# Kernel tuning notes

Measured on AMD Instinct MI355X. Metric: run time of the kernel, lower is better.

Reference implementation:

```python
import jax, jax.numpy as jnp
import numpy as np

N_EXPERTS = 8
N_ACTIVE = 2
DIM = 1024
HID = 2816
B, S = 4, 2048
W_SCALE = 0.02  # keep activations numerically tame


def setup_inputs() -> dict:
    key = jax.random.key(0)
    ks = jax.random.split(key, 9)
    return {
        "x": jax.random.normal(ks[0], (B, S, DIM), dtype=jnp.float32),
        "router_w": jax.random.normal(ks[1], (N_EXPERTS, DIM), dtype=jnp.float32) * W_SCALE,
        "expert_bias": jnp.zeros((N_EXPERTS,), dtype=jnp.float32),
        "gate_w": jax.random.normal(ks[2], (N_EXPERTS, HID, DIM), dtype=jnp.float32) * W_SCALE,
        "up_w": jax.random.normal(ks[3], (N_EXPERTS, HID, DIM), dtype=jnp.float32) * W_SCALE,
        "down_w": jax.random.normal(ks[4], (N_EXPERTS, DIM, HID), dtype=jnp.float32) * W_SCALE,
        "shared_gate_w": jax.random.normal(ks[5], (HID, DIM), dtype=jnp.float32) * W_SCALE,
        "shared_up_w": jax.random.normal(ks[6], (HID, DIM), dtype=jnp.float32) * W_SCALE,
        "shared_down_w": jax.random.normal(ks[7], (DIM, HID), dtype=jnp.float32) * W_SCALE,
    }


def _swiglu(x, gw, uw, dw):
    # x: [T, D]; gw/uw: [H, D]; dw: [D, H]
    return (jax.nn.silu(x @ gw.T) * (x @ uw.T)) @ dw.T


def reference(x, router_w, expert_bias, gate_w, up_w, down_w,
              shared_gate_w, shared_up_w, shared_down_w):
    bsz, seqlen, dim = x.shape
    x_flat = x.reshape(-1, dim)  # [T, D]

    # sigmoid router with auxfree bias, top-k selection
    logits = (x_flat @ router_w.T).astype(jnp.float32) + expert_bias  # [T, E]
    scores = jax.nn.sigmoid(logits)
    topk_scores, topk_idx = jax.lax.top_k(scores, N_ACTIVE)  # [T, K]
    topk_w = topk_scores / (jnp.sum(topk_scores, axis=-1, keepdims=True) + 1e-6)

    out = jnp.zeros_like(x_flat)
    # fixed small loop over experts; weight is 0 for unselected tokens,
    # which is mathematically identical to the masked gather/scatter in torch.
    for e in range(N_EXPERTS):
        w_e = jnp.sum(topk_w * (topk_idx == e), axis=-1)  # [T]
        y_e = _swiglu(x_flat, gate_w[e], up_w[e], down_w[e])  # [T, D]
        out = out + w_e[:, None].astype(x_flat.dtype) * y_e

    out = out + _swiglu(x_flat, shared_gate_w, shared_up_w, shared_down_w)
    return out.reshape(bsz, seqlen, dim)
```

## Files before the change

kernel.cpp:

```cpp
#include <hip/hip_runtime.h>
#include <hip/hip_bf16.h>
#include <stdint.h>

#define T_TOK  8192
#define DIM_   1024
#define HID_   2816
#define NEXP   8

typedef __bf16 bf16x8 __attribute__((ext_vector_type(8)));
typedef float  f32x4  __attribute__((ext_vector_type(4)));

__device__ __forceinline__ unsigned short f2bf(float f) {
  uint32_t u = __float_as_uint(f);
  u += 0x7FFFu + ((u >> 16) & 1u);
  return (unsigned short)(u >> 16);
}

__device__ __forceinline__ void gld_lds16(const void* g, void* l) {
  __builtin_amdgcn_global_load_lds(
      (const __attribute__((address_space(1))) uint32_t*)g,
      (__attribute__((address_space(3))) uint32_t*)l, 16, 0, 0);
}

__device__ __forceinline__ int lds_idx(int row, int col) {
  return row * 64 + ((((col >> 3) ^ (row & 7)) & 7) << 3);
}

__global__ __launch_bounds__(256) void cast_x_kernel(const float* __restrict__ in,
                                                     unsigned short* __restrict__ out) {
  int i = (blockIdx.x * 256 + threadIdx.x) * 8;
#pragma unroll
  for (int half = 0; half < 2; ++half) {
    float4 a = *reinterpret_cast<const float4*>(in + i + half * 4);
    ushort4 h4;
    h4.x = f2bf(a.x); h4.y = f2bf(a.y); h4.z = f2bf(a.z); h4.w = f2bf(a.w);
    *reinterpret_cast<ushort4*>(out + i + half * 4) = h4;
  }
}

__global__ __launch_bounds__(256) void cast_w_kernel(const float* __restrict__ in,
                                                     unsigned short* __restrict__ out) {
  size_t i = ((size_t)blockIdx.x * 256 + threadIdx.x) * 8;
#pragma unroll
  for (int half = 0; half < 2; ++half) {
    float4 a = *reinterpret_cast<const float4*>(in + i + half * 4);
    ushort4 h4;
    h4.x = f2bf(a.x); h4.y = f2bf(a.y); h4.z = f2bf(a.z); h4.w = f2bf(a.w);
    *reinterpret_cast<ushort4*>(out + i + half * 4) = h4;
  }
}

__global__ __launch_bounds__(256) void router_kernel(
    const float* __restrict__ x, const float* __restrict__ rw,
    const float* __restrict__ bias, int* __restrict__ cnt,
    int* __restrict__ list, float* __restrict__ wlist) {
  __shared__ float rws[NEXP * DIM_];
  for (int i = threadIdx.x; i < NEXP * DIM_ / 4; i += 256)
    reinterpret_cast<float4*>(rws)[i] = reinterpret_cast<const float4*>(rw)[i];
  __syncthreads();
  int wave = threadIdx.x >> 6, lane = threadIdx.x & 63;
  int t = blockIdx.x * 4 + wave;
  const float* xr = x + (size_t)t * DIM_;
  float p[NEXP];
#pragma unroll
  for (int e = 0; e < NEXP; ++e) p[e] = 0.f;
  for (int i = 0; i < DIM_ / 64; ++i) {
    float xv = xr[i * 64 + lane];
#pragma unroll
    for (int e = 0; e < NEXP; ++e) p[e] += xv * rws[e * DIM_ + i * 64 + lane];
  }
#pragma unroll
  for (int e = 0; e < NEXP; ++e) {
#pragma unroll
    for (int s = 32; s > 0; s >>= 1) p[e] += __shfl_xor(p[e], s);
  }
  if (lane == 0) {
    float sc[NEXP];
#pragma unroll
    for (int e = 0; e < NEXP; ++e) sc[e] = 1.f / (1.f + __expf(-(p[e] + bias[e])));
    int e0 = 0; float s0 = sc[0];
#pragma unroll
    for (int e = 1; e < NEXP; ++e) if (sc[e] > s0) { s0 = sc[e]; e0 = e; }
    int e1 = -1; float s1 = -1.f;
#pragma unroll
    for (int e = 0; e < NEXP; ++e) if (e != e0 && sc[e] > s1) { s1 = sc[e]; e1 = e; }
    float inv = 1.f / (s0 + s1 + 1e-6f);
    int p0 = atomicAdd(&cnt[e0], 1);
    list[e0 * T_TOK + p0] = t; wlist[e0 * T_TOK + p0] = s0 * inv;
    int p1 = atomicAdd(&cnt[e1], 1);
    list[e1 * T_TOK + p1] = t; wlist[e1 * T_TOK + p1] = s1 * inv;
  }
}

__global__ void scan_kernel(const int* __restrict__ cnt, int* __restrict__ off) {
  if (threadIdx.x == 0) {
    int a = 0;
#pragma unroll
    for (int e = 0; e < NEXP; ++e) { off[e] = a; a += cnt[e]; }
  }
}

template <bool EXPERT, bool WBF16>
__global__ __launch_bounds__(512) void gateup_k(
    const unsigned short* __restrict__ xbf,
    const void* __restrict__ gw_, const void* __restrict__ uw_,
    const int* __restrict__ cnt, const int* __restrict__ off,
    const int* __restrict__ list, unsigned short* __restrict__ hout) {
  const int e = EXPERT ? blockIdx.z : 0;
  const int cnt_e = EXPERT ? cnt[e] : T_TOK;
  const int bn = blockIdx.x, mb = blockIdx.y;
  if (mb * 128 >= cnt_e) return;
  const int rowoff = EXPERT ? off[e] : 0;

  __shared__ unsigned short As[128 * 64];
  __shared__ unsigned short Bg[128 * 64];
  __shared__ unsigned short Bu[128 * 64];

  const int tid = threadIdx.x;
  const size_t eoff = EXPERT ? (size_t)e * HID_ * DIM_ : 0;
  const unsigned short* gwb = WBF16 ? (const unsigned short*)gw_ + eoff : nullptr;
  const unsigned short* uwb = WBF16 ? (const unsigned short*)uw_ + eoff : nullptr;
  const float* gwf = WBF16 ? nullptr : (const float*)gw_ + eoff;
  const float* uwf = WBF16 ? nullptr : (const float*)uw_ + eoff;

  size_t arow[2], brow[2];
#pragma unroll
  for (int j = 0; j < 2; ++j) {
    int c = tid + j * 512;
    int r = c >> 3;
    int u = (c & 7) ^ (r & 7);
    int rl = mb * 128 + r;
    int gr;
    if (EXPERT) { int cl = rl < cnt_e ? rl : cnt_e - 1; gr = list[e * T_TOK + cl]; }
    else gr = rl;
    arow[j] = (size_t)gr * DIM_ + (size_t)(u * 8);
    brow[j] = (size_t)(bn * 128 + r) * DIM_ + (size_t)(u * 8);
  }
  size_t brow4[4];
  int bwr4[4];
  if (!WBF16) {
#pragma unroll
    for (int j = 0; j < 4; ++j) {
      int f = tid + j * 512;
      int rb = f >> 4, s = f & 15;
      bwr4[j] = rb * 64 + (((s >> 1) ^ (rb & 7)) * 2 + (s & 1)) * 4;
      brow4[j] = (size_t)(bn * 128 + rb) * DIM_ + (size_t)(s * 4);
    }
  }

  const f32x4 vzero = {0.f, 0.f, 0.f, 0.f};
  f32x4 accg[4][2], accu[4][2];
#pragma unroll
  for (int m = 0; m < 4; ++m)
#pragma unroll
    for (int n = 0; n < 2; ++n) { accg[m][n] = vzero; accu[m][n] = vzero; }

  const int wid = tid >> 6, lane = tid & 63;
  const int wm = wid >> 2, wn = wid & 3;
  const int fr = lane & 15, fk = (lane >> 4) * 8;

  for (int k0 = 0; k0 < DIM_; k0 += 64) {
    __syncthreads();
#pragma unroll
    for (int j = 0; j < 2; ++j) {
      int c = tid + j * 512;
      gld_lds16(xbf + arow[j] + k0, &As[c * 8]);
      if (WBF16) {
        gld_lds16(gwb + brow[j] + k0, &Bg[c * 8]);
        gld_lds16(uwb + brow[j] + k0, &Bu[c * 8]);
      }
    }
    if (!WBF16) {
#pragma unroll
      for (int j = 0; j < 4; ++j) {
        float4 vg = *reinterpret_cast<const float4*>(gwf + brow4[j] + k0);
        float4 vu = *reinterpret_cast<const float4*>(uwf + brow4[j] + k0);
        ushort4 wg; wg.x = f2bf(vg.x); wg.y = f2bf(vg.y); wg.z = f2bf(vg.z); wg.w = f2bf(vg.w);
        ushort4 wu; wu.x = f2bf(vu.x); wu.y = f2bf(vu.y); wu.z = f2bf(vu.z); wu.w = f2bf(vu.w);
        *reinterpret_cast<ushort4*>(&Bg[bwr4[j]]) = wg;
        *reinterpret_cast<ushort4*>(&Bu[bwr4[j]]) = wu;
      }
    }
    __syncthreads();
#pragma unroll
    for (int kk = 0; kk < 64; kk += 32) {
      bf16x8 a[4], bg[2], bu[2];
#pragma unroll
      for (int m = 0; m < 4; ++m) {
        int ar = wm * 64 + m * 16 + fr;
        a[m] = *reinterpret_cast<const bf16x8*>(&As[lds_idx(ar, kk + fk)]);
      }
#pragma unroll
      for (int n = 0; n < 2; ++n) {
        int br = wn * 32 + n * 16 + fr;
        bg[n] = *reinterpret_cast<const bf16x8*>(&Bg[lds_idx(br, kk + fk)]);
        bu[n] = *reinterpret_cast<const bf16x8*>(&Bu[lds_idx(br, kk + fk)]);
      }
#pragma unroll
      for (int m = 0; m < 4; ++m)
#pragma unroll
        for (int n = 0; n < 2; ++n) {
          accg[m][n] = __builtin_amdgcn_mfma_f32_16x16x32_bf16(a[m], bg[n], accg[m][n], 0, 0, 0);
          accu[m][n] = __builtin_amdgcn_mfma_f32_16x16x32_bf16(a[m], bu[n], accu[m][n], 0, 0, 0);
        }
    }
  }

  const int rb = mb * 128 + wm * 64 + (lane >> 4) * 4;
  const int cb = bn * 128 + wn * 32 + fr;
#pragma unroll
  for (int m = 0; m < 4; ++m) {
#pragma unroll
    for (int r = 0; r < 4; ++r) {
      int rl = rb + m * 16 + r;
      if (EXPERT && rl >= cnt_e) continue;
      size_t rowbase = (size_t)(rowoff + rl) * HID_ + cb;
#pragma unroll
      for (int n = 0; n < 2; ++n) {
        float g = accg[m][n][r], u = accu[m][n][r];
        float hv = (g / (1.f + __expf(-g))) * u;
        hout[rowbase + n * 16] = f2bf(hv);
      }
    }
  }
}

template <bool EXPERT, bool WBF16>
__global__ __launch_bounds__(512) void down_k(
    const unsigned short* __restrict__ h, const void* __restrict__ dw_,
    const int* __restrict__ cnt, const int* __restrict__ off,
    const int* __restrict__ list, const float* __restrict__ wlist,
    float* __restrict__ out) {
  const int e = EXPERT ? blockIdx.z : 0;
  const int cnt_e = EXPERT ? cnt[e] : T_TOK;
  const int bn = blockIdx.x, mb = blockIdx.y;
  if (mb * 128 >= cnt_e) return;
  const int rowoff = EXPERT ? off[e] : 0;

  __shared__ unsigned short As[128 * 64];
  __shared__ unsigned short Bs[128 * 64];

  const int tid = threadIdx.x;
  const size_t eoff = EXPERT ? (size_t)e * DIM_ * HID_ : 0;
  const unsigned short* dwb = WBF16 ? (const unsigned short*)dw_ + eoff : nullptr;
  const float* dwf = WBF16 ? nullptr : (const float*)dw_ + eoff;

  size_t arow[2], brow[2];
#pragma unroll
  for (int j = 0; j < 2; ++j) {
    int c = tid + j * 512;
    int r = c >> 3;
    int u = (c & 7) ^ (r & 7);
    int rl = mb * 128 + r;
    int cl = (EXPERT && rl >= cnt_e) ? cnt_e - 1 : rl;
    arow[j] = (size_t)(rowoff + cl) * HID_ + (size_t)(u * 8);
    brow[j] = (size_t)(bn * 128 + r) * HID_ + (size_t)(u * 8);
  }
  size_t brow4[4];
  int bwr4[4];
  if (!WBF16) {
#pragma unroll
    for (int j = 0; j < 4; ++j) {
      int f = tid + j * 512;
      int rb = f >> 4, s = f & 15;
      bwr4[j] = rb * 64 + (((s >> 1) ^ (rb & 7)) * 2 + (s & 1)) * 4;
      brow4[j] = (size_t)(bn * 128 + rb) * HID_ + (size_t)(s * 4);
    }
  }

  const f32x4 vzero = {0.f, 0.f, 0.f, 0.f};
  f32x4 acc[4][2];
#pragma unroll
  for (int m = 0; m < 4; ++m)
#pragma unroll
    for (int n = 0; n < 2; ++n) acc[m][n] = vzero;

  const int wid = tid >> 6, lane = tid & 63;
  const int wm = wid >> 2, wn = wid & 3;
  const int fr = lane & 15, fk = (lane >> 4) * 8;

  for (int k0 = 0; k0 < HID_; k0 += 64) {
    __syncthreads();
#pragma unroll
    for (int j = 0; j < 2; ++j) {
      int c = tid + j * 512;
      gld_lds16(h + arow[j] + k0, &As[c * 8]);
      if (WBF16) gld_lds16(dwb + brow[j] + k0, &Bs[c * 8]);
    }
    if (!WBF16) {
#pragma unroll
      for (int j = 0; j < 4; ++j) {
        float4 v = *reinterpret_cast<const float4*>(dwf + brow4[j] + k0);
        ushort4 w; w.x = f2bf(v.x); w.y = f2bf(v.y); w.z = f2bf(v.z); w.w = f2bf(v.w);
        *reinterpret_cast<ushort4*>(&Bs[bwr4[j]]) = w;
      }
    }
    __syncthreads();
#pragma unroll
    for (int kk = 0; kk < 64; kk += 32) {
      bf16x8 a[4], b[2];
#pragma unroll
      for (int m = 0; m < 4; ++m) {
        int ar = wm * 64 + m * 16 + fr;
        a[m] = *reinterpret_cast<const bf16x8*>(&As[lds_idx(ar, kk + fk)]);
      }
#pragma unroll
      for (int n = 0; n < 2; ++n) {
        int br = wn * 32 + n * 16 + fr;
        b[n] = *reinterpret_cast<const bf16x8*>(&Bs[lds_idx(br, kk + fk)]);
      }
#pragma unroll
      for (int m = 0; m < 4; ++m)
#pragma unroll
        for (int n = 0; n < 2; ++n)
          acc[m][n] = __builtin_amdgcn_mfma_f32_16x16x32_bf16(a[m], b[n], acc[m][n], 0, 0, 0);
    }
  }

  const int rb = mb * 128 + wm * 64 + (lane >> 4) * 4;
  const int cb = bn * 128 + wn * 32 + fr;
#pragma unroll
  for (int m = 0; m < 4; ++m) {
#pragma unroll
    for (int r = 0; r < 4; ++r) {
      int rl = rb + m * 16 + r;
      if (EXPERT && rl >= cnt_e) continue;
      int tok; float w;
      if (EXPERT) { tok = list[e * T_TOK + rl]; w = wlist[e * T_TOK + rl]; }
      else { tok = rl; w = 1.f; }
      float* orow = out + (size_t)tok * DIM_ + cb;
#pragma unroll
      for (int n = 0; n < 2; ++n)
        atomicAdd(orow + n * 16, w * acc[m][n][r]);
    }
  }
}

extern "C" void kernel_launch(void* const* d_in, const int* in_sizes, int n_in,
                              void* d_out, int out_size, void* d_ws, size_t ws_size,
                              hipStream_t stream) {
  const float* x    = (const float*)d_in[0];
  const float* rw   = (const float*)d_in[1];
  const float* bias = (const float*)d_in[2];
  const float* gw   = (const float*)d_in[3];
  const float* uw   = (const float*)d_in[4];
  const float* dwn  = (const float*)d_in[5];
  const float* sgw  = (const float*)d_in[6];
  const float* suw  = (const float*)d_in[7];
  const float* sdw  = (const float*)d_in[8];
  float* out = (float*)d_out;

  char* ws = (char*)d_ws;
  size_t o = 0;
  auto alloc = [&](size_t b) { size_t r = o; o = (o + b + 255) & ~(size_t)255; return r; };
  unsigned short* xbf = (unsigned short*)(ws + alloc((size_t)T_TOK * DIM_ * 2));
  unsigned short* h   = (unsigned short*)(ws + alloc(((size_t)2 * T_TOK + 128) * HID_ * 2));
  int*   cnt   = (int*)(ws + alloc(NEXP * 4));
  int*   off   = (int*)(ws + alloc(NEXP * 4));
  int*   list  = (int*)(ws + alloc((size_t)NEXP * T_TOK * 4));
  float* wlist = (float*)(ws + alloc((size_t)NEXP * T_TOK * 4));
  const size_t need_base = o;
  const size_t WE = (size_t)HID_ * DIM_;
  unsigned short* gwb  = (unsigned short*)(ws + alloc(NEXP * WE * 2));
  unsigned short* uwb  = (unsigned short*)(ws + alloc(NEXP * WE * 2));
  const bool pcGU = (o <= ws_size);
  unsigned short* dwb  = (unsigned short*)(ws + alloc(NEXP * WE * 2));
  const bool pcDN = (o <= ws_size);
  unsigned short* sgwb = (unsigned short*)(ws + alloc(WE * 2));
  unsigned short* suwb = (unsigned short*)(ws + alloc(WE * 2));
  unsigned short* sdwb = (unsigned short*)(ws + alloc(WE * 2));
  const bool pcSH = (o <= ws_size);
  if (need_base > ws_size) {
    hipMemsetAsync(d_out, 0, (size_t)out_size * 4, stream);
    return;
  }

  hipMemsetAsync(out, 0, (size_t)out_size * 4, stream);
  hipMemsetAsync(cnt, 0, NEXP * 4, stream);
  cast_x_kernel<<<T_TOK * DIM_ / 8 / 256, 256, 0, stream>>>(x, xbf);
  router_kernel<<<T_TOK / 4, 256, 0, stream>>>(x, rw, bias, cnt, list, wlist);
  scan_kernel<<<1, 64, 0, stream>>>(cnt, off);

  const int WB = (int)(NEXP * WE / 2048);
  const int WS = (int)(WE / 2048);
  if (pcGU) {
    cast_w_kernel<<<WB, 256, 0, stream>>>(gw, gwb);
    cast_w_kernel<<<WB, 256, 0, stream>>>(uw, uwb);
  }
  if (pcDN) cast_w_kernel<<<WB, 256, 0, stream>>>(dwn, dwb);
  if (pcSH) {
    cast_w_kernel<<<WS, 256, 0, stream>>>(sgw, sgwb);
    cast_w_kernel<<<WS, 256, 0, stream>>>(suw, suwb);
    cast_w_kernel<<<WS, 256, 0, stream>>>(sdw, sdwb);
  }

  if (pcSH) {
    gateup_k<false, true><<<dim3(HID_ / 128, T_TOK / 128, 1), 512, 0, stream>>>(
        xbf, sgwb, suwb, cnt, off, list, h);
    down_k<false, true><<<dim3(DIM_ / 128, T_TOK / 128, 1), 512, 0, stream>>>(
        h, sdwb, cnt, off, list, wlist, out);
  } else {
    gateup_k<false, false><<<dim3(HID_ / 128, T_TOK / 128, 1), 512, 0, stream>>>(
        xbf, sgw, suw, cnt, off, list, h);
    down_k<false, false><<<dim3(DIM_ / 128, T_TOK / 128, 1), 512, 0, stream>>>(
        h, sdw, cnt, off, list, wlist, out);
  }
  if (pcGU)
    gateup_k<true, true><<<dim3(HID_ / 128, T_TOK / 128, NEXP), 512, 0, stream>>>(
        xbf, gwb, uwb, cnt, off, list, h);
  else
    gateup_k<true, false><<<dim3(HID_ / 128, T_TOK / 128, NEXP), 512, 0, stream>>>(
        xbf, gw, uw, cnt, off, list, h);
  if (pcDN)
    down_k<true, true><<<dim3(DIM_ / 128, T_TOK / 128, NEXP), 512, 0, stream>>>(
        h, dwb, cnt, off, list, wlist, out);
  else
    down_k<true, false><<<dim3(DIM_ / 128, T_TOK / 128, NEXP), 512, 0, stream>>>(
        h, dwn, cnt, off, list, wlist, out);
}
```

Measured before the change: 1.086 ms.

## Widen GEMM N-tiles to 256, drop fp32 weight fallback, store shared output directly

The gate/up kernel now runs 1024-thread blocks covering 256 hidden columns per tile, and the down kernel covers 256 output columns with a 4x4 fragment tile per wave. The goal is more reuse of each loaded A tile and fewer blocks. The shared-expert down pass writes its output with plain stores instead of atomics, which also removes the memset of the output. The fp32-weight fallback paths are removed, so the kernel now requires enough workspace for all bf16 weight copies. The cost is higher LDS and register use per block, which may lower occupancy.

```diff
diff --git a/kernel.cpp b/kernel.cpp
--- a/kernel.cpp
+++ b/kernel.cpp
@@ -100,10 +100,10 @@
   }
 }
 
-template <bool EXPERT, bool WBF16>
-__global__ __launch_bounds__(512) void gateup_k(
+template <bool EXPERT>
+__global__ __launch_bounds__(1024) void gateup_k(
     const unsigned short* __restrict__ xbf,
-    const void* __restrict__ gw_, const void* __restrict__ uw_,
+    const unsigned short* __restrict__ gwb_, const unsigned short* __restrict__ uwb_,
     const int* __restrict__ cnt, const int* __restrict__ off,
     const int* __restrict__ list, unsigned short* __restrict__ hout) {
   const int e = EXPERT ? blockIdx.z : 0;
@@ -113,39 +113,32 @@
   const int rowoff = EXPERT ? off[e] : 0;
 
   __shared__ unsigned short As[128 * 64];
-  __shared__ unsigned short Bg[128 * 64];
-  __shared__ unsigned short Bu[128 * 64];
+  __shared__ unsigned short Bg[256 * 64];
+  __shared__ unsigned short Bu[256 * 64];
 
   const int tid = threadIdx.x;
   const size_t eoff = EXPERT ? (size_t)e * HID_ * DIM_ : 0;
-  const unsigned short* gwb = WBF16 ? (const unsigned short*)gw_ + eoff : nullptr;
-  const unsigned short* uwb = WBF16 ? (const unsigned short*)uw_ + eoff : nullptr;
-  const float* gwf = WBF16 ? nullptr : (const float*)gw_ + eoff;
-  const float* uwf = WBF16 ? nullptr : (const float*)uw_ + eoff;
-
-  size_t arow[2], brow[2];
-#pragma unroll
-  for (int j = 0; j < 2; ++j) {
-    int c = tid + j * 512;
+  const unsigned short* gwb = gwb_ + eoff;
+  const unsigned short* uwb = uwb_ + eoff;
+
+  size_t arow;
+  {
+    int c = tid;
     int r = c >> 3;
     int u = (c & 7) ^ (r & 7);
     int rl = mb * 128 + r;
     int gr;
     if (EXPERT) { int cl = rl < cnt_e ? rl : cnt_e - 1; gr = list[e * T_TOK + cl]; }
     else gr = rl;
-    arow[j] = (size_t)gr * DIM_ + (size_t)(u * 8);
-    brow[j] = (size_t)(bn * 128 + r) * DIM_ + (size_t)(u * 8);
-  }
-  size_t brow4[4];
-  int bwr4[4];
-  if (!WBF16) {
-#pragma unroll
-    for (int j = 0; j < 4; ++j) {
-      int f = tid + j * 512;
-      int rb = f >> 4, s = f & 15;
-      bwr4[j] = rb * 64 + (((s >> 1) ^ (rb & 7)) * 2 + (s & 1)) * 4;
-      brow4[j] = (size_t)(bn * 128 + rb) * DIM_ + (size_t)(s * 4);
-    }
+    arow = (size_t)gr * DIM_ + (size_t)(u * 8);
+  }
+  size_t brow[2];
+#pragma unroll
+  for (int j = 0; j < 2; ++j) {
+    int c = tid + j * 1024;
+    int r = c >> 3;
+    int u = (c & 7) ^ (r & 7);
+    brow[j] = (size_t)(bn * 256 + r) * DIM_ + (size_t)(u * 8);
   }
 
   const f32x4 vzero = {0.f, 0.f, 0.f, 0.f};
@@ -156,30 +149,17 @@
     for (int n = 0; n < 2; ++n) { accg[m][n] = vzero; accu[m][n] = vzero; }
 
   const int wid = tid >> 6, lane = tid & 63;
-  const int wm = wid >> 2, wn = wid & 3;
+  const int wm = wid >> 3, wn = wid & 7;
   const int fr = lane & 15, fk = (lane >> 4) * 8;
 
   for (int k0 = 0; k0 < DIM_; k0 += 64) {
     __syncthreads();
+    gld_lds16(xbf + arow + k0, &As[tid * 8]);
 #pragma unroll
     for (int j = 0; j < 2; ++j) {
-      int c = tid + j * 512;
-      gld_lds16(xbf + arow[j] + k0, &As[c * 8]);
-      if (WBF16) {
-        gld_lds16(gwb + brow[j] + k0, &Bg[c * 8]);
-        gld_lds16(uwb + brow[j] + k0, &Bu[c * 8]);
-      }
-    }
-    if (!WBF16) {
-#pragma unroll
-      for (int j = 0; j < 4; ++j) {
-        float4 vg = *reinterpret_cast<const float4*>(gwf + brow4[j] + k0);
-        float4 vu = *reinterpret_cast<const float4*>(uwf + brow4[j] + k0);
-        ushort4 wg; wg.x = f2bf(vg.x); wg.y = f2bf(vg.y); wg.z = f2bf(vg.z); wg.w = f2bf(vg.w);
-        ushort4 wu; wu.x = f2bf(vu.x); wu.y = f2bf(vu.y); wu.z = f2bf(vu.z); wu.w = f2bf(vu.w);
-        *reinterpret_cast<ushort4*>(&Bg[bwr4[j]]) = wg;
-        *reinterpret_cast<ushort4*>(&Bu[bwr4[j]]) = wu;
-      }
+      int c = tid + j * 1024;
+      gld_lds16(gwb + brow[j] + k0, &Bg[c * 8]);
+      gld_lds16(uwb + brow[j] + k0, &Bu[c * 8]);
     }
     __syncthreads();
 #pragma unroll
@@ -207,7 +187,7 @@
   }
 
   const int rb = mb * 128 + wm * 64 + (lane >> 4) * 4;
-  const int cb = bn * 128 + wn * 32 + fr;
+  const int cb = bn * 256 + wn * 32 + fr;
 #pragma unroll
   for (int m = 0; m < 4; ++m) {
 #pragma unroll
@@ -225,9 +205,9 @@
   }
 }
 
-template <bool EXPERT, bool WBF16>
+template <bool EXPERT>
 __global__ __launch_bounds__(512) void down_k(
-    const unsigned short* __restrict__ h, const void* __restrict__ dw_,
+    const unsigned short* __restrict__ h, const unsigned short* __restrict__ dwb_,
     const int* __restrict__ cnt, const int* __restrict__ off,
     const int* __restrict__ list, const float* __restrict__ wlist,
     float* __restrict__ out) {
@@ -238,14 +218,12 @@
   const int rowoff = EXPERT ? off[e] : 0;
 
   __shared__ unsigned short As[128 * 64];
-  __shared__ unsigned short Bs[128 * 64];
+  __shared__ unsigned short Bs[256 * 64];
 
   const int tid = threadIdx.x;
-  const size_t eoff = EXPERT ? (size_t)e * DIM_ * HID_ : 0;
-  const unsigned short* dwb = WBF16 ? (const unsigned short*)dw_ + eoff : nullptr;
-  const float* dwf = WBF16 ? nullptr : (const float*)dw_ + eoff;
-
-  size_t arow[2], brow[2];
+  const unsigned short* dwb = dwb_ + (EXPERT ? (size_t)e * DIM_ * HID_ : 0);
+
+  size_t arow[2];
 #pragma unroll
   for (int j = 0; j < 2; ++j) {
     int c = tid + j * 512;
@@ -254,26 +232,22 @@
     int rl = mb * 128 + r;
     int cl = (EXPERT && rl >= cnt_e) ? cnt_e - 1 : rl;
     arow[j] = (size_t)(rowoff + cl) * HID_ + (size_t)(u * 8);
-    brow[j] = (size_t)(bn * 128 + r) * HID_ + (size_t)(u * 8);
-  }
-  size_t brow4[4];
-  int bwr4[4];
-  if (!WBF16) {
-#pragma unroll
-    for (int j = 0; j < 4; ++j) {
-      int f = tid + j * 512;
-      int rb = f >> 4, s = f & 15;
-      bwr4[j] = rb * 64 + (((s >> 1) ^ (rb & 7)) * 2 + (s & 1)) * 4;
-      brow4[j] = (size_t)(bn * 128 + rb) * HID_ + (size_t)(s * 4);
-    }
+  }
+  size_t brow[4];
+#pragma unroll
+  for (int j = 0; j < 4; ++j) {
+    int c = tid + j * 512;
+    int r = c >> 3;
+    int u = (c & 7) ^ (r & 7);
+    brow[j] = (size_t)(bn * 256 + r) * HID_ + (size_t)(u * 8);
   }
 
   const f32x4 vzero = {0.f, 0.f, 0.f, 0.f};
-  f32x4 acc[4][2];
+  f32x4 acc[4][4];
 #pragma unroll
   for (int m = 0; m < 4; ++m)
 #pragma unroll
-    for (int n = 0; n < 2; ++n) acc[m][n] = vzero;
+    for (int n = 0; n < 4; ++n) acc[m][n] = vzero;
 
   const int wid = tid >> 6, lane = tid & 63;
   const int wm = wid >> 2, wn = wid & 3;
@@ -285,53 +259,55 @@
     for (int j = 0; j < 2; ++j) {
       int c = tid + j * 512;
       gld_lds16(h + arow[j] + k0, &As[c * 8]);
-      if (WBF16) gld_lds16(dwb + brow[j] + k0, &Bs[c * 8]);
-    }
-    if (!WBF16) {
-#pragma unroll
-      for (int j = 0; j < 4; ++j) {
-        float4 v = *reinterpret_cast<const float4*>(dwf + brow4[j] + k0);
-        ushort4 w; w.x = f2bf(v.x); w.y = f2bf(v.y); w.z = f2bf(v.z); w.w = f2bf(v.w);
-        *reinterpret_cast<ushort4*>(&Bs[bwr4[j]]) = w;
-      }
+    }
+#pragma unroll
+    for (int j = 0; j < 4; ++j) {
+      int c = tid + j * 512;
+      gld_lds16(dwb + brow[j] + k0, &Bs[c * 8]);
     }
     __syncthreads();
 #pragma unroll
     for (int kk = 0; kk < 64; kk += 32) {
-      bf16x8 a[4], b[2];
+      bf16x8 a[4], b[4];
 #pragma unroll
       for (int m = 0; m < 4; ++m) {
         int ar = wm * 64 + m * 16 + fr;
         a[m] = *reinterpret_cast<const bf16x8*>(&As[lds_idx(ar, kk + fk)]);
       }
 #pragma unroll
-      for (int n = 0; n < 2; ++n) {
-        int br = wn * 32 + n * 16 + fr;
+      for (int n = 0; n < 4; ++n) {
+        int br = wn * 64 + n * 16 + fr;
         b[n] = *reinterpret_cast<const bf16x8*>(&Bs[lds_idx(br, kk + fk)]);
       }
 #pragma unroll
       for (int m = 0; m < 4; ++m)
 #pragma unroll
-        for (int n = 0; n < 2; ++n)
+        for (int n = 0; n < 4; ++n)
           acc[m][n] = __builtin_amdgcn_mfma_f32_16x16x32_bf16(a[m], b[n], acc[m][n], 0, 0, 0);
     }
   }
 
   const int rb = mb * 128 + wm * 64 + (lane >> 4) * 4;
-  const int cb = bn * 128 + wn * 32 + fr;
+  const int cb = bn * 256 + wn * 64 + fr;
 #pragma unroll
   for (int m = 0; m < 4; ++m) {
 #pragma unroll
     for (int r = 0; r < 4; ++r) {
       int rl = rb + m * 16 + r;
       if (EXPERT && rl >= cnt_e) continue;
-      int tok; float w;
-      if (EXPERT) { tok = list[e * T_TOK + rl]; w = wlist[e * T_TOK + rl]; }
-      else { tok = rl; w = 1.f; }
-      float* orow = out + (size_t)tok * DIM_ + cb;
-#pragma unroll
-      for (int n = 0; n < 2; ++n)
-        atomicAdd(orow + n * 16, w * acc[m][n][r]);
+      if (EXPERT) {
+        int tok = list[e * T_TOK + rl];
+        float w = wlist[e * T_TOK + rl];
+        float* orow = out + (size_t)tok * DIM_ + cb;
+#pragma unroll
+        for (int n = 0; n < 4; ++n)
+          atomicAdd(orow + n * 16, w * acc[m][n][r]);
+      } else {
+        float* orow = out + (size_t)rl * DIM_ + cb;
+#pragma unroll
+        for (int n = 0; n < 4; ++n)
+          orow[n * 16] = acc[m][n][r];
+      }
     }
   }
 }
@@ -359,23 +335,18 @@
   int*   off   = (int*)(ws + alloc(NEXP * 4));
   int*   list  = (int*)(ws + alloc((size_t)NEXP * T_TOK * 4));
   float* wlist = (float*)(ws + alloc((size_t)NEXP * T_TOK * 4));
-  const size_t need_base = o;
   const size_t WE = (size_t)HID_ * DIM_;
   unsigned short* gwb  = (unsigned short*)(ws + alloc(NEXP * WE * 2));
   unsigned short* uwb  = (unsigned short*)(ws + alloc(NEXP * WE * 2));
-  const bool pcGU = (o <= ws_size);
   unsigned short* dwb  = (unsigned short*)(ws + alloc(NEXP * WE * 2));
-  const bool pcDN = (o <= ws_size);
   unsigned short* sgwb = (unsigned short*)(ws + alloc(WE * 2));
   unsigned short* suwb = (unsigned short*)(ws + alloc(WE * 2));
   unsigned short* sdwb = (unsigned short*)(ws + alloc(WE * 2));
-  const bool pcSH = (o <= ws_size);
-  if (need_base > ws_size) {
+  if (o > ws_size) {
     hipMemsetAsync(d_out, 0, (size_t)out_size * 4, stream);
     return;
   }
 
-  hipMemsetAsync(out, 0, (size_t)out_size * 4, stream);
   hipMemsetAsync(cnt, 0, NEXP * 4, stream);
   cast_x_kernel<<<T_TOK * DIM_ / 8 / 256, 256, 0, stream>>>(x, xbf);
   router_kernel<<<T_TOK / 4, 256, 0, stream>>>(x, rw, bias, cnt, list, wlist);
@@ -383,38 +354,19 @@
 
   const int WB = (int)(NEXP * WE / 2048);
   const int WS = (int)(WE / 2048);
-  if (pcGU) {
-    cast_w_kernel<<<WB, 256, 0, stream>>>(gw, gwb);
-    cast_w_kernel<<<WB, 256, 0, stream>>>(uw, uwb);
-  }
-  if (pcDN) cast_w_kernel<<<WB, 256, 0, stream>>>(dwn, dwb);
-  if (pcSH) {
-    cast_w_kernel<<<WS, 256, 0, stream>>>(sgw, sgwb);
-    cast_w_kernel<<<WS, 256, 0, stream>>>(suw, suwb);
-    cast_w_kernel<<<WS, 256, 0, stream>>>(sdw, sdwb);
-  }
-
-  if (pcSH) {
-    gateup_k<false, true><<<dim3(HID_ / 128, T_TOK / 128, 1), 512, 0, stream>>>(
-        xbf, sgwb, suwb, cnt, off, list, h);
-    down_k<false, true><<<dim3(DIM_ / 128, T_TOK / 128, 1), 512, 0, stream>>>(
-        h, sdwb, cnt, off, list, wlist, out);
-  } else {
-    gateup_k<false, false><<<dim3(HID_ / 128, T_TOK / 128, 1), 512, 0, stream>>>(
-        xbf, sgw, suw, cnt, off, list, h);
-    down_k<false, false><<<dim3(DIM_ / 128, T_TOK / 128, 1), 512, 0, stream>>>(
-        h, sdw, cnt, off, list, wlist, out);
-  }
-  if (pcGU)
-    gateup_k<true, true><<<dim3(HID_ / 128, T_TOK / 128, NEXP), 512, 0, stream>>>(
-        xbf, gwb, uwb, cnt, off, list, h);
-  else
-    gateup_k<true, false><<<dim3(HID_ / 128, T_TOK / 128, NEXP), 512, 0, stream>>>(
-        xbf, gw, uw, cnt, off, list, h);
-  if (pcDN)
-    down_k<true, true><<<dim3(DIM_ / 128, T_TOK / 128, NEXP), 512, 0, stream>>>(
-        h, dwb, cnt, off, list, wlist, out);
-  else
-    down_k<true, false><<<dim3(DIM_ / 128, T_TOK / 128, NEXP), 512, 0, stream>>>(
-        h, dwn, cnt, off, list, wlist, out);
-}
+  cast_w_kernel<<<WB, 256, 0, stream>>>(gw,  gwb);
+  cast_w_kernel<<<WB, 256, 0, stream>>>(uw,  uwb);
+  cast_w_kernel<<<WB, 256, 0, stream>>>(dwn, dwb);
+  cast_w_kernel<<<WS, 256, 0, stream>>>(sgw, sgwb);
+  cast_w_kernel<<<WS, 256, 0, stream>>>(suw, suwb);
+  cast_w_kernel<<<WS, 256, 0, stream>>>(sdw, sdwb);
+
+  gateup_k<false><<<dim3(HID_ / 256, T_TOK / 128, 1), 1024, 0, stream>>>(
+      xbf, sgwb, suwb, cnt, off, list, h);
+  down_k<false><<<dim3(DIM_ / 256, T_TOK / 128, 1), 512, 0, stream>>>(
+      h, sdwb, cnt, off, list, wlist, out);
+  gateup_k<true><<<dim3(HID_ / 256, T_TOK / 128, NEXP), 1024, 0, stream>>>(
+      xbf, gwb, uwb, cnt, off, list, h);
+  down_k<true><<<dim3(DIM_ / 256, T_TOK / 128, NEXP), 512, 0, stream>>>(
+      h, dwb, cnt, off, list, wlist, out);
+}
```

After: 1.225 ms. +12.8%, slower.
